# Kernel tuning notes

Measured on AMD Instinct MI355X. Metric: run time of the kernel, lower is better.

The kernel has to match this reference:

```python
import jax, jax.numpy as jnp
import numpy as np

B, T, D = 4, 4096, 1024


def setup_inputs() -> dict:
    key = jax.random.key(0)
    ks = jax.random.split(key, 10)
    scale = 1.0 / np.sqrt(D)
    x = jax.random.normal(ks[0], (B, T, D), jnp.float32)
    last_x = jnp.zeros((D,), jnp.float32)
    last_num = jnp.zeros((D,), jnp.float32)
    last_den = jnp.zeros((D,), jnp.float32)
    time_decay = jax.random.normal(ks[1], (D,), jnp.float32) * 0.1
    time_first = jax.random.normal(ks[2], (D,), jnp.float32) * 0.1
    time_mix_k = jax.random.uniform(ks[3], (1, 1, D), jnp.float32)
    time_mix_v = jax.random.uniform(ks[4], (1, 1, D), jnp.float32)
    time_mix_r = jax.random.uniform(ks[5], (1, 1, D), jnp.float32)
    Wk = jax.random.normal(ks[6], (D, D), jnp.float32) * scale
    Wv = jax.random.normal(ks[7], (D, D), jnp.float32) * scale
    Wr = jax.random.normal(ks[8], (D, D), jnp.float32) * scale
    Wo = jax.random.normal(ks[9], (D, D), jnp.float32) * scale
    return {"x": x, "last_x": last_x, "last_num": last_num, "last_den": last_den,
            "time_decay": time_decay, "time_first": time_first,
            "time_mix_k": time_mix_k, "time_mix_v": time_mix_v, "time_mix_r": time_mix_r,
            "Wk": Wk, "Wv": Wv, "Wr": Wr, "Wo": Wo}


def reference(x, last_x, last_num, last_den, time_decay, time_first,
              time_mix_k, time_mix_v, time_mix_r, Wk, Wv, Wr, Wo):
    # token-shift lerps against the incoming state (broadcast over B, T)
    k = jnp.einsum('btd,ed->bte', x * time_mix_k + last_x * (1.0 - time_mix_k), Wk)
    v = jnp.einsum('btd,ed->bte', x * time_mix_v + last_x * (1.0 - time_mix_v), Wv)
    r = jnp.einsum('btd,ed->bte', x * time_mix_r + last_x * (1.0 - time_mix_r), Wr)
    # WKV numerics, exactly as the original (no extra stabilization)
    efk = jnp.exp(time_first + k)          # exp(time_first + k), [B,T,D]
    wkv = (last_num + efk * v) / (last_den + efk)
    rwkv = jax.nn.sigmoid(r) * wkv
    decay = jnp.exp(-jnp.exp(time_decay))  # [D]
    ek = jnp.exp(k)
    num = decay * last_num + ek * v
    den = decay * last_den + ek
    out = jnp.einsum('btd,ed->bte', rwkv, Wo)
    return out, x[..., -1, :], num[..., -1, :], den[..., -1, :]
```

## Files before the change

### kernel.cpp

```cpp
#include <hip/hip_runtime.h>
#include <cstdint>
#include <cstddef>

constexpr int DD = 1024;
constexpr int TT = 4096;
constexpr int BB = 4;
constexpr int MM = BB * TT;

typedef __bf16 bf16x8 __attribute__((ext_vector_type(8)));
typedef float  f32x4  __attribute__((ext_vector_type(4)));

__device__ __forceinline__ unsigned short f2bf(float f) {
  union { float f; uint32_t u; } c; c.f = f;
  uint32_t r = (c.u + 0x7FFFu + ((c.u >> 16) & 1u)) >> 16;
  return (unsigned short)r;
}

__device__ __forceinline__ float fast_rcp(float x) {
  return __builtin_amdgcn_rcpf(x);
}

__device__ __forceinline__ void async_ld16(const unsigned short* g, unsigned short* lds_dst) {
  __builtin_amdgcn_global_load_lds(
      (const __attribute__((address_space(1))) void*)g,
      (__attribute__((address_space(3))) void*)lds_dst,
      16, 0, 0);
}

__global__ void prep_all(const float* __restrict__ Wk, const float* __restrict__ Wv,
                         const float* __restrict__ Wr, const float* __restrict__ Wo,
                         const float* __restrict__ tmk, const float* __restrict__ tmv,
                         const float* __restrict__ tmr,
                         const float* __restrict__ last_x,
                         const float4* __restrict__ x,
                         unsigned short* __restrict__ wz,
                         unsigned short* __restrict__ wo,
                         float* __restrict__ bias,
                         ushort4* __restrict__ xb,
                         float4* __restrict__ out_xlast) {
  if (blockIdx.x < 1024) {
    int w = (blockIdx.x * 256 + threadIdx.x) >> 6;
    int lane = threadIdx.x & 63;
    int z = w >> 10;
    int e = w & (DD - 1);
    const float* W  = (z == 0) ? Wk  : (z == 1) ? Wv  : (z == 2) ? Wr : Wo;
    const float* tm = (z == 0) ? tmk : (z == 1) ? tmv : tmr;
    unsigned short* dst = (z < 3) ? (wz + (size_t)z * DD * DD + (size_t)e * DD)
                                  : (wo + (size_t)e * DD);
    float s = 0.f;
#pragma unroll
    for (int j = 0; j < 4; ++j) {
      int d = j * 256 + lane * 4;
      float4 wv4 = *(const float4*)(W + (size_t)e * DD + d);
      if (z < 3) {
        float4 t4 = *(const float4*)(tm + d);
        float4 l4 = *(const float4*)(last_x + d);
        s += l4.x * (1.f - t4.x) * wv4.x + l4.y * (1.f - t4.y) * wv4.y +
             l4.z * (1.f - t4.z) * wv4.z + l4.w * (1.f - t4.w) * wv4.w;
        wv4.x *= t4.x; wv4.y *= t4.y; wv4.z *= t4.z; wv4.w *= t4.w;
      }
      ushort4 o;
      o.x = f2bf(wv4.x); o.y = f2bf(wv4.y); o.z = f2bf(wv4.z); o.w = f2bf(wv4.w);
      *(ushort4*)(dst + d) = o;
    }
    if (z < 3) {
      for (int off = 32; off; off >>= 1) s += __shfl_down(s, off, 64);
      if (lane == 0) bias[z * DD + e] = s;
    }
  } else {
    int i = (blockIdx.x - 1024) * 256 + threadIdx.x;
    float4 v = x[i];
    ushort4 o;
    o.x = f2bf(v.x); o.y = f2bf(v.y); o.z = f2bf(v.z); o.w = f2bf(v.w);
    xb[i] = o;
    int m = i >> 8;
    if ((m & (TT - 1)) == (TT - 1)) {
      int b = m >> 12;
      out_xlast[b * 256 + (i & 255)] = v;
    }
  }
}

__global__ __launch_bounds__(256, 2) void gemm_kvr(
    const unsigned short* __restrict__ A,
    const unsigned short* __restrict__ Wz,
    const float* __restrict__ bias,
    const float* __restrict__ time_first, const float* __restrict__ time_decay,
    const float* __restrict__ last_num, const float* __restrict__ last_den,
    unsigned short* __restrict__ rwkv,
    float* __restrict__ out_num, float* __restrict__ out_den) {
  __shared__ unsigned short lA[2][128 * 32];
  __shared__ unsigned short lB[2][3][64 * 32];
  const int tid  = threadIdx.x;
  const int lane = tid & 63;
  const int wave = tid >> 6;

  const int id  = blockIdx.y * gridDim.x + blockIdx.x;
  const int xcd = id & 7;
  const int s   = id >> 3;
  const int m0 = (xcd * 16 + (s >> 4)) * 128;
  const int n0 = (s & 15) * 64;

  const int wm = (wave >> 1) * 64;
  const int wn = (wave & 1) * 32;

  f32x4 acc[3][4][2] = {};

  const int fr_row = lane & 15;
  const int fr_kb  = (lane >> 4) * 16;
  const int srow = tid >> 2;
  const int scol = (tid & 3) * 8;

  for (int k0 = 0; k0 < DD; k0 += 64) {
    __syncthreads();
#pragma unroll
    for (int h = 0; h < 2; ++h) {
      int kk = k0 + h * 32;
#pragma unroll
      for (int it = 0; it < 2; ++it) {
        int cc  = it * 256 + tid;
        int row = cc >> 2;
        async_ld16(A + (size_t)(m0 + row) * DD + (kk + scol),
                   lA[h] + (size_t)(it * 256 + wave * 64) * 8);
      }
#pragma unroll
      for (int z = 0; z < 3; ++z) {
        async_ld16(Wz + (size_t)z * DD * DD + (size_t)(n0 + srow) * DD + (kk + scol),
                   lB[h][z] + (size_t)(wave * 64) * 8);
      }
    }
    __syncthreads();

#pragma unroll
    for (int h = 0; h < 2; ++h) {
      bf16x8 af[4], bfr[3][2];
#pragma unroll
      for (int i = 0; i < 4; ++i)
        af[i] = *(const bf16x8*)((const char*)lA[h] + ((wm + i * 16 + fr_row) * 64 + fr_kb));
#pragma unroll
      for (int z = 0; z < 3; ++z)
#pragma unroll
        for (int j = 0; j < 2; ++j)
          bfr[z][j] = *(const bf16x8*)((const char*)lB[h][z] + ((wn + j * 16 + fr_row) * 64 + fr_kb));

#pragma unroll
      for (int mi = 0; mi < 4; ++mi)
#pragma unroll
        for (int z = 0; z < 3; ++z)
#pragma unroll
          for (int ni = 0; ni < 2; ++ni)
            acc[z][mi][ni] = __builtin_amdgcn_mfma_f32_16x16x32_bf16(
                af[mi], bfr[z][ni], acc[z][mi][ni], 0, 0, 0);
    }
  }

  const int crow = (lane >> 4) * 4;
  const int ccol = lane & 15;
#pragma unroll
  for (int ni = 0; ni < 2; ++ni) {
    int gnz = n0 + wn + ni * 16 + ccol;
    float bk = bias[gnz], bv = bias[DD + gnz], br = bias[2 * DD + gnz];
    float tf = time_first[gnz];
    float ln = last_num[gnz], ld = last_den[gnz];
    float dec = __expf(-__expf(time_decay[gnz]));
#pragma unroll
    for (int mi = 0; mi < 4; ++mi) {
#pragma unroll
      for (int r = 0; r < 4; ++r) {
        int gm = m0 + wm + mi * 16 + crow + r;
        float kk = acc[0][mi][ni][r] + bk;
        float vv = acc[1][mi][ni][r] + bv;
        float rr = acc[2][mi][ni][r] + br;
        float efk = __expf(tf + kk);
        float wkv = (ln + efk * vv) * fast_rcp(ld + efk);
        float sr  = fast_rcp(1.0f + __expf(-rr));
        rwkv[(size_t)gm * DD + gnz] = f2bf(sr * wkv);
        if ((gm & (TT - 1)) == (TT - 1)) {
          int b = gm >> 12;
          float ek = __expf(kk);
          out_num[b * DD + gnz] = dec * ln + ek * vv;
          out_den[b * DD + gnz] = dec * ld + ek;
        }
      }
    }
  }
}

__global__ void gemm_bt128(const unsigned short* __restrict__ A,
                           const unsigned short* __restrict__ Bw,
                           float* __restrict__ Cf,
                           int M, int N, int K) {
  __shared__ unsigned short lA[2][128 * 32];
  __shared__ unsigned short lB[2][128 * 32];
  const int tid  = threadIdx.x;
  const int lane = tid & 63;
  const int wave = tid >> 6;

  const int nBlocks = N >> 7;
  const int mBlocks = M >> 7;
  const int id  = blockIdx.y * gridDim.x + blockIdx.x;
  const int xcd = id & 7;
  const int s   = id >> 3;
  const int mPer = mBlocks >> 3;
  const int m0 = (xcd * mPer + s / nBlocks) * 128;
  const int n0 = (s % nBlocks) * 128;

  const int wm = (wave >> 1) * 64;
  const int wn = (wave & 1) * 64;

  f32x4 acc[4][4] = {};
  const int fr_row = lane & 15;
  const int fr_kb  = (lane >> 4) * 16;
  const int scol = (tid & 3) * 8;

  for (int k0 = 0; k0 < K; k0 += 64) {
    __syncthreads();
#pragma unroll
    for (int h = 0; h < 2; ++h) {
      int kk = k0 + h * 32;
#pragma unroll
      for (int it = 0; it < 2; ++it) {
        int cc  = it * 256 + tid;
        int row = cc >> 2;
        async_ld16(A + (size_t)(m0 + row) * K + (kk + scol),
                   lA[h] + (size_t)(it * 256 + wave * 64) * 8);
      }
#pragma unroll
      for (int it = 0; it < 2; ++it) {
        int cc  = it * 256 + tid;
        int row = cc >> 2;
        async_ld16(Bw + (size_t)(n0 + row) * K + (kk + scol),
                   lB[h] + (size_t)(it * 256 + wave * 64) * 8);
      }
    }
    __syncthreads();

#pragma unroll
    for (int h = 0; h < 2; ++h) {
      bf16x8 af[4], bfr[4];
#pragma unroll
      for (int i = 0; i < 4; ++i) {
        af[i]  = *(const bf16x8*)((const char*)lA[h] + ((wm + i * 16 + fr_row) * 64 + fr_kb));
        bfr[i] = *(const bf16x8*)((const char*)lB[h] + ((wn + i * 16 + fr_row) * 64 + fr_kb));
      }
#pragma unroll
      for (int mi = 0; mi < 4; ++mi)
#pragma unroll
        for (int ni = 0; ni < 4; ++ni)
          acc[mi][ni] = __builtin_amdgcn_mfma_f32_16x16x32_bf16(af[mi], bfr[ni], acc[mi][ni], 0, 0, 0);
    }
  }

  const int crow = (lane >> 4) * 4;
  const int ccol = lane & 15;
#pragma unroll
  for (int mi = 0; mi < 4; ++mi) {
#pragma unroll
    for (int ni = 0; ni < 4; ++ni) {
      int gn = n0 + wn + ni * 16 + ccol;
#pragma unroll
      for (int r = 0; r < 4; ++r) {
        int gm = m0 + wm + mi * 16 + crow + r;
        Cf[(size_t)gm * N + gn] = acc[mi][ni][r];
      }
    }
  }
}

extern "C" void kernel_launch(void* const* d_in, const int* in_sizes, int n_in,
                              void* d_out, int out_size, void* d_ws, size_t ws_size,
                              hipStream_t stream) {
  const float* x          = (const float*)d_in[0];
  const float* last_x     = (const float*)d_in[1];
  const float* last_num   = (const float*)d_in[2];
  const float* last_den   = (const float*)d_in[3];
  const float* time_decay = (const float*)d_in[4];
  const float* time_first = (const float*)d_in[5];
  const float* tmk        = (const float*)d_in[6];
  const float* tmv        = (const float*)d_in[7];
  const float* tmr        = (const float*)d_in[8];
  const float* Wk         = (const float*)d_in[9];
  const float* Wv         = (const float*)d_in[10];
  const float* Wr         = (const float*)d_in[11];
  const float* Wo         = (const float*)d_in[12];

  float* out       = (float*)d_out;
  float* out_xlast = out + (size_t)MM * DD;
  float* out_num   = out_xlast + BB * DD;
  float* out_den   = out_num + BB * DD;

  char* ws = (char*)d_ws;
  unsigned short* xb   = (unsigned short*)ws;
  unsigned short* wz   = (unsigned short*)(ws + 33554432);
  unsigned short* wo   = (unsigned short*)(ws + 39845888);
  float*          bias = (float*)(ws + 41943040);
  unsigned short* rwkv = (unsigned short*)(ws + 41955328);

  prep_all<<<1024 + MM * DD / 4 / 256, 256, 0, stream>>>(
      Wk, Wv, Wr, Wo, tmk, tmv, tmr, last_x, (const float4*)x,
      wz, wo, bias, (ushort4*)xb, (float4*)out_xlast);

  gemm_kvr<<<dim3(DD / 64, MM / 128), 256, 0, stream>>>(
      xb, wz, bias, time_first, time_decay, last_num, last_den,
      rwkv, out_num, out_den);

  gemm_bt128<<<dim3(DD / 128, MM / 128), 256, 0, stream>>>(
      rwkv, wo, out, MM, DD, DD);
}
```

Measured before the change: 291.5 us.

## Rewrite output projection GEMM as 256x256 tile with 4-stage async pipeline

```diff
diff --git a/kernel.cpp b/kernel.cpp
--- a/kernel.cpp
+++ b/kernel.cpp
@@ -26,6 +26,12 @@
       (__attribute__((address_space(3))) void*)lds_dst,
       16, 0, 0);
 }
+
+#define VWAIT(n) asm volatile("s_waitcnt vmcnt(" #n ")" ::: "memory")
+#define LWAIT0() asm volatile("s_waitcnt lgkmcnt(0)" ::: "memory")
+#define SB()     __builtin_amdgcn_sched_barrier(0)
+
+__device__ __forceinline__ int swzb(int b) { return b ^ (((b >> 9) & 1) << 5); }
 
 __global__ void prep_all(const float* __restrict__ Wk, const float* __restrict__ Wv,
                          const float* __restrict__ Wr, const float* __restrict__ Wo,
@@ -186,75 +192,122 @@
   }
 }
 
-__global__ void gemm_bt128(const unsigned short* __restrict__ A,
-                           const unsigned short* __restrict__ Bw,
-                           float* __restrict__ Cf,
-                           int M, int N, int K) {
-  __shared__ unsigned short lA[2][128 * 32];
-  __shared__ unsigned short lB[2][128 * 32];
+__global__ __launch_bounds__(512, 2) void gemm_bt256(
+    const unsigned short* __restrict__ A,
+    const unsigned short* __restrict__ Bw,
+    float* __restrict__ Cf,
+    int M, int N, int K) {
+  __shared__ __align__(1024) unsigned short sA[4][256 * 32];
+  __shared__ __align__(1024) unsigned short sB[4][256 * 32];
   const int tid  = threadIdx.x;
   const int lane = tid & 63;
   const int wave = tid >> 6;
 
-  const int nBlocks = N >> 7;
-  const int mBlocks = M >> 7;
   const int id  = blockIdx.y * gridDim.x + blockIdx.x;
   const int xcd = id & 7;
   const int s   = id >> 3;
-  const int mPer = mBlocks >> 3;
-  const int m0 = (xcd * mPer + s / nBlocks) * 128;
-  const int n0 = (s % nBlocks) * 128;
-
-  const int wm = (wave >> 1) * 64;
-  const int wn = (wave & 1) * 64;
-
-  f32x4 acc[4][4] = {};
-  const int fr_row = lane & 15;
-  const int fr_kb  = (lane >> 4) * 16;
-  const int scol = (tid & 3) * 8;
-
-  for (int k0 = 0; k0 < K; k0 += 64) {
-    __syncthreads();
-#pragma unroll
-    for (int h = 0; h < 2; ++h) {
-      int kk = k0 + h * 32;
-#pragma unroll
-      for (int it = 0; it < 2; ++it) {
-        int cc  = it * 256 + tid;
-        int row = cc >> 2;
-        async_ld16(A + (size_t)(m0 + row) * K + (kk + scol),
-                   lA[h] + (size_t)(it * 256 + wave * 64) * 8);
-      }
-#pragma unroll
-      for (int it = 0; it < 2; ++it) {
-        int cc  = it * 256 + tid;
-        int row = cc >> 2;
-        async_ld16(Bw + (size_t)(n0 + row) * K + (kk + scol),
-                   lB[h] + (size_t)(it * 256 + wave * 64) * 8);
-      }
-    }
-    __syncthreads();
-
-#pragma unroll
-    for (int h = 0; h < 2; ++h) {
-      bf16x8 af[4], bfr[4];
-#pragma unroll
-      for (int i = 0; i < 4; ++i) {
-        af[i]  = *(const bf16x8*)((const char*)lA[h] + ((wm + i * 16 + fr_row) * 64 + fr_kb));
-        bfr[i] = *(const bf16x8*)((const char*)lB[h] + ((wn + i * 16 + fr_row) * 64 + fr_kb));
-      }
-#pragma unroll
-      for (int mi = 0; mi < 4; ++mi)
-#pragma unroll
-        for (int ni = 0; ni < 4; ++ni)
-          acc[mi][ni] = __builtin_amdgcn_mfma_f32_16x16x32_bf16(af[mi], bfr[ni], acc[mi][ni], 0, 0, 0);
-    }
-  }
-
-  const int crow = (lane >> 4) * 4;
-  const int ccol = lane & 15;
-#pragma unroll
-  for (int mi = 0; mi < 4; ++mi) {
+  const int m0 = (xcd * 8 + (s >> 2)) * 256;
+  const int n0 = (s & 3) * 256;
+
+  const int wm = (wave >> 2) * 128;
+  const int wn = (wave & 3) * 64;
+  const int fr = lane & 15;
+  const int fq = lane >> 4;
+
+  int phA[8], phB[4];
+#pragma unroll
+  for (int mi = 0; mi < 8; ++mi)
+    phA[mi] = swzb((wm + mi * 16 + fr) * 64 + fq * 16);
+#pragma unroll
+  for (int ni = 0; ni < 4; ++ni)
+    phB[ni] = swzb((wn + ni * 16 + fr) * 64 + fq * 16);
+
+  size_t aSrc[2], bSrc[2]; int dPl[2];
+#pragma unroll
+  for (int u = 0; u < 2; ++u) {
+    int plane = u * 8 + wave;
+    dPl[u] = plane * 1024;
+    int pb = plane * 1024 + lane * 16;
+    int lq = swzb(pb);
+    int r = lq >> 6, cb = lq & 63;
+    aSrc[u] = (size_t)(m0 + r) * K + (cb >> 1);
+    bSrc[u] = (size_t)(n0 + r) * K + (cb >> 1);
+  }
+  auto stageA = [&](int slot, int t) {
+    const int kk = t * 32;
+#pragma unroll
+    for (int u = 0; u < 2; ++u)
+      async_ld16(A + aSrc[u] + kk, (unsigned short*)((char*)sA[slot] + dPl[u]));
+  };
+  auto stageB = [&](int slot, int t) {
+    const int kk = t * 32;
+#pragma unroll
+    for (int u = 0; u < 2; ++u)
+      async_ld16(Bw + bSrc[u] + kk, (unsigned short*)((char*)sB[slot] + dPl[u]));
+  };
+
+  f32x4 acc[8][4] = {};
+  const int nt = K >> 5;
+
+  stageA(0, 0); stageB(0, 0);
+  stageA(1, 1); stageB(1, 1);
+  stageA(2, 2); stageB(2, 2);
+  VWAIT(8); SB();
+  __builtin_amdgcn_s_barrier();
+
+#pragma unroll 1
+  for (int t = 0; t < nt; ++t) {
+    const int slot = t & 3;
+
+    bf16x8 af0[4], bf[4];
+#pragma unroll
+    for (int mi = 0; mi < 4; ++mi)
+      af0[mi] = *(const bf16x8*)((const char*)sA[slot] + phA[mi]);
+#pragma unroll
+    for (int ni = 0; ni < 4; ++ni)
+      bf[ni] = *(const bf16x8*)((const char*)sB[slot] + phB[ni]);
+    if (t < nt - 3) stageA((t + 3) & 3, t + 3);
+    __builtin_amdgcn_s_barrier();
+    LWAIT0(); SB();
+    __builtin_amdgcn_s_setprio(1);
+#pragma unroll
+    for (int mi = 0; mi < 4; ++mi)
+#pragma unroll
+      for (int ni = 0; ni < 4; ++ni)
+        acc[mi][ni] = __builtin_amdgcn_mfma_f32_16x16x32_bf16(
+            af0[mi], bf[ni], acc[mi][ni], 0, 0, 0);
+    __builtin_amdgcn_s_setprio(0);
+    __builtin_amdgcn_s_barrier();
+
+    bf16x8 af1[4];
+#pragma unroll
+    for (int mi = 0; mi < 4; ++mi)
+      af1[mi] = *(const bf16x8*)((const char*)sA[slot] + phA[4 + mi]);
+    if (t < nt - 3) stageB((t + 3) & 3, t + 3);
+    __builtin_amdgcn_s_barrier();
+    LWAIT0(); SB();
+    __builtin_amdgcn_s_setprio(1);
+#pragma unroll
+    for (int mi = 0; mi < 4; ++mi)
+#pragma unroll
+      for (int ni = 0; ni < 4; ++ni)
+        acc[4 + mi][ni] = __builtin_amdgcn_mfma_f32_16x16x32_bf16(
+            af1[mi], bf[ni], acc[4 + mi][ni], 0, 0, 0);
+    __builtin_amdgcn_s_setprio(0);
+
+    if (t < nt - 1) {
+      if (t < nt - 3)       VWAIT(8);
+      else if (t == nt - 3) VWAIT(4);
+      else                  VWAIT(0);
+      SB();
+      __builtin_amdgcn_s_barrier();
+    }
+  }
+
+  const int crow = fq * 4;
+  const int ccol = fr;
+#pragma unroll
+  for (int mi = 0; mi < 8; ++mi) {
 #pragma unroll
     for (int ni = 0; ni < 4; ++ni) {
       int gn = n0 + wn + ni * 16 + ccol;
@@ -304,6 +357,6 @@
       xb, wz, bias, time_first, time_decay, last_num, last_den,
       rwkv, out_num, out_den);
 
-  gemm_bt128<<<dim3(DD / 128, MM / 128), 256, 0, stream>>>(
+  gemm_bt256<<<dim3(DD / 256, MM / 256), 512, 0, stream>>>(
       rwkv, wo, out, MM, DD, DD);
 }
```

New measurement: 293.2 us. About the same (+0.6%).
